# Kernel tuning notes

Measured on AMD Instinct MI355X. Metric: run time of the kernel, lower is better.

The kernel has to match this reference:

```python
import jax, jax.numpy as jnp
import numpy as np

THRESHOLD = 0.35      # overlap_thresh
NEGPOS_RATIO = 7
VAR0, VAR1 = 0.1, 0.2  # self.variance


def make_priors():
    # Standard RetinaFace 640x640 anchor grid -> 16800 priors (cx, cy, w, h)
    img = 640
    steps = [8, 16, 32]
    min_sizes = [[16, 32], [64, 128], [256, 512]]
    out = []
    for step, ms in zip(steps, min_sizes):
        f = img // step
        ii, jj = np.meshgrid(np.arange(f), np.arange(f), indexing="ij")
        cx = ((jj + 0.5) * step / img).ravel().astype(np.float32)
        cy = ((ii + 0.5) * step / img).ravel().astype(np.float32)
        for m in ms:
            s = np.full_like(cx, m / img)
            out.append(np.stack([cx, cy, s, s], axis=-1))
    return jnp.asarray(np.concatenate(out, axis=0), dtype=jnp.float32)


def jaccard(a, b):
    # a: [O,4] point-form gt boxes, b: [P,4] point-form priors -> IoU [O,P]
    lt = jnp.maximum(a[:, None, :2], b[None, :, :2])
    rb = jnp.minimum(a[:, None, 2:], b[None, :, 2:])
    wh = jnp.clip(rb - lt, 0.0)
    inter = wh[..., 0] * wh[..., 1]
    area_a = ((a[:, 2] - a[:, 0]) * (a[:, 3] - a[:, 1]))[:, None]
    area_b = ((b[:, 2] - b[:, 0]) * (b[:, 3] - b[:, 1]))[None, :]
    return inter / (area_a + area_b - inter)


def setup_inputs() -> dict:
    key = jax.random.key(0)
    ks = jax.random.split(key, 7)
    B, P, O = 64, 16800, 64
    loc_data = jax.random.normal(ks[0], (B, P, 4), jnp.float32)
    conf_data = jax.random.normal(ks[1], (B, P, 2), jnp.float32)
    landm_data = jax.random.normal(ks[2], (B, P, 10), jnp.float32)
    priors = make_priors()
    # targets: [B, O, 15] = [xmin ymin xmax ymax | 10 landmark coords | label]
    c = jax.random.uniform(ks[3], (B, O, 2), minval=0.15, maxval=0.85)
    wh = jax.random.uniform(ks[4], (B, O, 2), minval=0.05, maxval=0.3)
    boxes = jnp.concatenate([jnp.clip(c - wh / 2, 1e-3, 0.999),
                             jnp.clip(c + wh / 2, 1e-3, 0.999)], axis=-1)
    landms = jax.random.uniform(ks[5], (B, O, 10))
    lab = jnp.where(jax.random.uniform(ks[6], (B, O, 1)) < 0.8, 1.0, -1.0)
    targets = jnp.concatenate([boxes, landms, lab], axis=-1).astype(jnp.float32)
    return {"loc_data": loc_data, "conf_data": conf_data,
            "landm_data": landm_data, "priors": priors, "targets": targets}


def _smooth_l1(x):
    ax = jnp.abs(x)
    return jnp.where(ax < 1.0, 0.5 * ax * ax, ax - 0.5)


def reference(loc_data, conf_data, landm_data, priors, targets):
    B, P, C = conf_data.shape
    O = targets.shape[1]
    priors_pf = jnp.concatenate([priors[:, :2] - priors[:, 2:] * 0.5,
                                 priors[:, :2] + priors[:, 2:] * 0.5], axis=1)

    def match_one(t):
        truths = t[:, :4]
        landms = t[:, 4:14]
        labels = t[:, 14].astype(jnp.int32)
        ov = jaccard(truths, priors_pf)               # [O,P]
        bp_ov = ov.max(axis=1)                         # best prior per truth
        bp_idx = jnp.argmax(ov, axis=1)
        valid = bp_ov >= 0.2                           # RetinaFace gt filter
        bt_ov = ov.max(axis=0)                         # best truth per prior
        bt_idx = jnp.argmax(ov, axis=0)
        # index_fill_(best_prior_idx, 2) for valid gts, ensure best prior kept
        bt_ov = bt_ov.at[bp_idx].set(jnp.where(valid, 2.0, bt_ov[bp_idx]))
        bt_idx = bt_idx.at[bp_idx].set(jnp.arange(O))
        matched = truths[bt_idx]                       # [P,4] point form
        conf = labels[bt_idx]
        conf = jnp.where(bt_ov < THRESHOLD, 0, conf)
        # encode loc target
        g_cxcy = ((matched[:, :2] + matched[:, 2:]) * 0.5 - priors[:, :2]) / (VAR0 * priors[:, 2:])
        g_wh = jnp.log((matched[:, 2:] - matched[:, :2]) / priors[:, 2:]) / VAR1
        loc = jnp.concatenate([g_cxcy, g_wh], axis=1)
        # encode landmark target (5 points)
        ml = landms[bt_idx].reshape(P, 5, 2)
        lm = ((ml - priors[:, None, :2]) / (VAR0 * priors[:, None, 2:])).reshape(P, 10)
        any_valid = jnp.any(valid)                     # early-return branch of match()
        return (jnp.where(any_valid, loc, 0.0),
                jnp.where(any_valid, conf, 0),
                jnp.where(any_valid, lm, 0.0))

    loc_t, conf_t, landm_t = jax.vmap(match_one)(targets)
    loc_t = jax.lax.stop_gradient(loc_t)       # targets built from .data in torch
    landm_t = jax.lax.stop_gradient(landm_t)

    # landmark loss over conf_t > 0
    pos1 = conf_t > 0
    N1 = jnp.maximum(pos1.sum().astype(jnp.float32), 1.0)
    loss_landm = jnp.sum(jnp.where(pos1[..., None], _smooth_l1(landm_data - landm_t), 0.0))

    # localization loss over conf_t != 0 (labels -1 and 1 both positive)
    pos = conf_t != 0
    conf_t1 = jnp.where(pos, 1, conf_t)        # conf_t[pos] = 1 -> values in {0,1}
    loss_l = jnp.sum(jnp.where(pos[..., None], _smooth_l1(loc_data - loc_t), 0.0))

    # hard negative mining
    lse = jax.nn.logsumexp(conf_data, axis=2)                       # [B,P]
    picked = jnp.take_along_axis(conf_data, conf_t1[..., None], axis=2)[..., 0]
    ce_all = lse - picked                                            # per-anchor CE
    rank_score = jnp.where(pos, 0.0, ce_all)
    loss_idx = jnp.argsort(-rank_score, axis=1)
    idx_rank = jnp.argsort(loss_idx, axis=1)
    num_pos = pos.sum(axis=1, keepdims=True)
    num_neg = jnp.minimum(NEGPOS_RATIO * num_pos, P - 1)
    neg = idx_rank < num_neg
    union = pos | neg
    loss_c = jnp.sum(jnp.where(union, ce_all, 0.0))

    N = jnp.maximum(num_pos.sum().astype(jnp.float32), 1.0)
    return loss_l / N, loss_c / N, loss_landm / N1
```

## Files before the change

### kernel.cpp

```cpp
#include <hip/hip_runtime.h>
#include <math.h>

#define B 64
#define P 16800
#define O 64
#define THRESH 0.35f
#define VALID_T 0.2f
#define HB 2048
#define HSHIFT 21
#define AREA_M 0.34f
#define CCAP 4096
#define MULT 4
#define CHB (MULT * 256)
#define NB2 ((P + CHB - 1) / CHB)
#define KD1B (B * NB2)
#define KB2B (B * O / 4)

__device__ __forceinline__ float smooth_l1(float x) {
    float ax = fabsf(x);
    return ax < 1.f ? 0.5f * ax * ax : ax - 0.5f;
}
__device__ __forceinline__ float lse2(float c0, float c1) {
    float m = fmaxf(c0, c1);
    return m + __logf(__expf(c0 - m) + __expf(c1 - m));
}
__device__ __forceinline__ void iou_upd(float4 t, float area_a,
                                        float px1, float py1, float px2, float py2,
                                        float area_b,
                                        float& bnum, float& bden, int& bio, int o) {
    float w = fmaxf(fminf(t.z, px2) - fmaxf(t.x, px1), 0.f);
    float h = fmaxf(fminf(t.w, py2) - fmaxf(t.y, py1), 0.f);
    float inter = w * h;
    float den = area_a + area_b - inter;
    if (inter * bden > bnum * den) { bnum = inter; bden = den; bio = o; }
}
__device__ __forceinline__ float wave_sum(float v) {
#pragma unroll
    for (int s = 32; s > 0; s >>= 1) v += __shfl_down(v, s, 64);
    return v;
}
__device__ __forceinline__ int wave_sum_i(int v) {
#pragma unroll
    for (int s = 32; s > 0; s >>= 1) v += __shfl_down(v, s, 64);
    return v;
}
__device__ __forceinline__ float wave_min(float v) {
#pragma unroll
    for (int s = 32; s > 0; s >>= 1) v = fminf(v, __shfl_xor(v, s, 64));
    return v;
}
__device__ __forceinline__ float wave_max(float v) {
#pragma unroll
    for (int s = 32; s > 0; s >>= 1) v = fmaxf(v, __shfl_xor(v, s, 64));
    return v;
}
__device__ __forceinline__ int wave_sufscan(int v, int lane) {
#pragma unroll
    for (int s = 1; s < 64; s <<= 1) {
        int o = __shfl_down(v, s, 64);
        if (lane + s < 64) v += o;
    }
    return v;
}

__global__ void __launch_bounds__(256) kMain(
        const float* __restrict__ loc_data, const float* __restrict__ conf_data,
        const float* __restrict__ landm_data, const float* __restrict__ priors,
        const float* __restrict__ targets,
        float* __restrict__ rank,
        int* __restrict__ num_pos, float* __restrict__ pos_ce,
        float* __restrict__ gsum, int* __restrict__ np1_tot,
        unsigned long long* __restrict__ bp_final) {
    if (blockIdx.x >= KD1B) {
        int pair = (blockIdx.x - KD1B) * 4 + (threadIdx.x >> 6);
        int lane = threadIdx.x & 63;
        int o = pair & (O - 1);
        int b = pair >> 6;
        const float* tt = &targets[(b * O + o) * 15];
        float tx1 = tt[0], ty1 = tt[1], tx2 = tt[2], ty2 = tt[3];
        float area_a = (tx2 - tx1) * (ty2 - ty1);
        float4 tb = make_float4(tx1, ty1, tx2, ty2);
        float bn = 0.f, bd = 1.f;
        unsigned bp = 0u;
        const int fs[6]   = {80, 80, 40, 40, 20, 20};
        const int ms[6]   = {16, 32, 64, 128, 256, 512};
        const int base[6] = {0, 6400, 12800, 14400, 16000, 16400};
#pragma unroll
        for (int c = 0; c < 6; ++c) {
            int f = fs[c];
            float inv = (float)f;
            float h = (float)ms[c] * (0.5f / 640.f);
            int j0 = (int)floorf((tx1 - h) * inv - 0.5f) - 1; if (j0 < 0) j0 = 0;
            int j1 = (int)ceilf((tx2 + h) * inv - 0.5f) + 1;  if (j1 > f - 1) j1 = f - 1;
            int i0 = (int)floorf((ty1 - h) * inv - 0.5f) - 1; if (i0 < 0) i0 = 0;
            int i1 = (int)ceilf((ty2 + h) * inv - 0.5f) + 1;  if (i1 > f - 1) i1 = f - 1;
            if (j1 < j0 || i1 < i0) continue;
            int nj = j1 - j0 + 1;
            int n = (i1 - i0 + 1) * nj;
            float rcp_nj = 1.0f / (float)nj;
            for (int idx = lane; idx < n; idx += 64) {
                int ii = (int)((float)idx * rcp_nj);
                int jj = idx - ii * nj;
                if (jj < 0) { ii--; jj += nj; } else if (jj >= nj) { ii++; jj -= nj; }
                int p = base[c] + (i0 + ii) * f + (j0 + jj);
                float4 q = ((const float4*)priors)[p];
                float px1 = q.x - q.z * 0.5f, py1 = q.y - q.w * 0.5f;
                float px2 = q.x + q.z * 0.5f, py2 = q.y + q.w * 0.5f;
                float areab = (px2 - px1) * (py2 - py1);
                float w = fmaxf(fminf(tb.z, px2) - fmaxf(tb.x, px1), 0.f);
                float hh = fmaxf(fminf(tb.w, py2) - fmaxf(tb.y, py1), 0.f);
                float inter = w * hh;
                float den = area_a + areab - inter;
                float l = bn * den, r = inter * bd;
                if (r > l) { bn = inter; bd = den; bp = (unsigned)p; }
            }
        }
#pragma unroll
        for (int s = 32; s > 0; s >>= 1) {
            float no = __shfl_xor(bn, s, 64), dd = __shfl_xor(bd, s, 64);
            unsigned po = __shfl_xor(bp, s, 64);
            float l = bn * dd, r = no * bd;
            bool take = (r > l) || (r == l && po < bp);
            if (take) { bn = no; bd = dd; bp = po; }
        }
        if (lane == 0) {
            float iou = bn / bd;
            bp_final[b * O + o] = ((unsigned long long)__float_as_uint(iou) << 32)
                                | (unsigned)(0xFFFFFFFFu - bp);
        }
        return;
    }
    int blk = blockIdx.x % NB2;
    int b = blockIdx.x / NB2;
    int p0 = blk * CHB;
    __shared__ float traw[O * 15];
    __shared__ float4 t4[O];
    __shared__ float ta[O], lab[O];
    __shared__ float4 wbb[4];
    __shared__ float2 wab[4];
    __shared__ int alist[O];
    __shared__ int s_cnt;
    __shared__ float wredf[3][4];
    __shared__ int wredi[2][4];
    int tid = threadIdx.x;
    if (tid < O * 15 / 4)
        ((float4*)traw)[tid] = ((const float4*)(targets + (size_t)b * O * 15))[tid];
    float px1[MULT], py1[MULT], px2[MULT], py2[MULT], areab[MULT];
    float4 pr4[MULT];
    float bnum[MULT], bden[MULT]; int bi[MULT]; bool act[MULT];
    float bx1 = 1e30f, by1 = 1e30f, bx2 = -1e30f, by2 = -1e30f;
    float amn = 1e30f, amx = -1e30f;
#pragma unroll
    for (int mi = 0; mi < MULT; ++mi) {
        int p = p0 + mi * 256 + tid;
        act[mi] = (p < P);
        int pc = act[mi] ? p : (P - 1);
        float4 q = ((const float4*)priors)[pc];
        pr4[mi] = q;
        px1[mi] = q.x - q.z * 0.5f; py1[mi] = q.y - q.w * 0.5f;
        px2[mi] = q.x + q.z * 0.5f; py2[mi] = q.y + q.w * 0.5f;
        areab[mi] = (px2[mi] - px1[mi]) * (py2[mi] - py1[mi]);
        bx1 = fminf(bx1, px1[mi]); by1 = fminf(by1, py1[mi]);
        bx2 = fmaxf(bx2, px2[mi]); by2 = fmaxf(by2, py2[mi]);
        amn = fminf(amn, areab[mi]); amx = fmaxf(amx, areab[mi]);
        bnum[mi] = 0.f; bden[mi] = 1.f; bi[mi] = 0;
    }
    bx1 = wave_min(bx1); by1 = wave_min(by1);
    bx2 = wave_max(bx2); by2 = wave_max(by2);
    amn = wave_min(amn); amx = wave_max(amx);
    int wid = tid >> 6, lid = tid & 63;
    if (lid == 0) { wbb[wid] = make_float4(bx1, by1, bx2, by2); wab[wid] = make_float2(amn, amx); }
    __syncthreads();
    if (tid < 64) {
        const float* tr = &traw[tid * 15];
        float a0 = tr[0], a1 = tr[1], a2 = tr[2], a3 = tr[3];
        float4 t = make_float4(a0, a1, a2, a3);
        t4[tid] = t;
        float Aa = (a2 - a0) * (a3 - a1);
        ta[tid] = Aa;
        lab[tid] = tr[14];
        float ux1 = fminf(fminf(wbb[0].x, wbb[1].x), fminf(wbb[2].x, wbb[3].x));
        float uy1 = fminf(fminf(wbb[0].y, wbb[1].y), fminf(wbb[2].y, wbb[3].y));
        float ux2 = fmaxf(fmaxf(wbb[0].z, wbb[1].z), fmaxf(wbb[2].z, wbb[3].z));
        float uy2 = fmaxf(fmaxf(wbb[0].w, wbb[1].w), fmaxf(wbb[2].w, wbb[3].w));
        float bmn = fminf(fminf(wab[0].x, wab[1].x), fminf(wab[2].x, wab[3].x));
        float bmx = fmaxf(fmaxf(wab[0].y, wab[1].y), fmaxf(wab[2].y, wab[3].y));
        bool pass = (fminf(t.z, ux2) - fmaxf(t.x, ux1) > 0.f) &&
                    (fminf(t.w, uy2) - fmaxf(t.y, uy1) > 0.f) &&
                    (Aa >= AREA_M * bmn) && (bmx >= AREA_M * Aa);
        unsigned long long mask = __ballot(pass);
        if (tid == 0) s_cnt = __popcll(mask);
        if (pass) {
            int pos = __popcll(mask & ((1ull << tid) - 1ull));
            alist[pos] = tid;
        }
    }
    __syncthreads();
    int cnt = s_cnt;
    for (int li = 0; li < cnt; ++li) {
        int o = alist[li];
        float4 t = t4[o];
        float w0 = fminf(t.z, bx2) - fmaxf(t.x, bx1);
        float h0 = fminf(t.w, by2) - fmaxf(t.y, by1);
        if (w0 <= 0.f || h0 <= 0.f) continue;
        float Aa = ta[o];
#pragma unroll
        for (int mi = 0; mi < MULT; ++mi) {
            float Ap = areab[mi];
            if (Aa >= AREA_M * Ap && Ap >= AREA_M * Aa)
                iou_upd(t, Aa, px1[mi], py1[mi], px2[mi], py2[mi], Ap,
                        bnum[mi], bden[mi], bi[mi], o);
        }
    }
    float ll = 0.f, llm = 0.f, cep = 0.f;
    int cp = 0, cp1 = 0;
#pragma unroll
    for (int mi = 0; mi < MULT; ++mi) {
        if (!act[mi]) continue;
        int p = p0 + mi * 256 + tid;
        float best = bnum[mi] / bden[mi];
        int conf = (best >= THRESH) ? (int)lab[bi[mi]] : 0;
        float2 c01 = ((const float2*)conf_data)[b * P + p];
        float c0 = c01.x, c1 = c01.y;
        float lse = lse2(c0, c1);
        bool pos = conf != 0;
        float ce = lse - (pos ? c1 : c0);
        float rv = pos ? 0.f : ce;
        rank[(size_t)b * P + p] = rv;
        if (pos) {
            cp++; cep += ce;
            int ti = bi[mi];
            float cx = pr4[mi].x, cy = pr4[mi].y, sw = pr4[mi].z, sh = pr4[mi].w;
            float4 t = t4[ti];
            float gx = ((t.x + t.z) * 0.5f - cx) / (0.1f * sw);
            float gy = ((t.y + t.w) * 0.5f - cy) / (0.1f * sh);
            float gw = logf((t.z - t.x) / sw) / 0.2f;
            float gh = logf((t.w - t.y) / sh) / 0.2f;
            const float* ld = &loc_data[(size_t)(b * P + p) * 4];
            ll += smooth_l1(ld[0] - gx) + smooth_l1(ld[1] - gy) +
                  smooth_l1(ld[2] - gw) + smooth_l1(ld[3] - gh);
            if (conf > 0) {
                cp1++;
                const float* lmd = &landm_data[(size_t)(b * P + p) * 10];
                const float* lmt = &traw[ti * 15 + 4];
                for (int k5 = 0; k5 < 5; ++k5) {
                    float lx = (lmt[k5 * 2 + 0] - cx) / (0.1f * sw);
                    float ly = (lmt[k5 * 2 + 1] - cy) / (0.1f * sh);
                    llm += smooth_l1(lmd[k5 * 2 + 0] - lx) + smooth_l1(lmd[k5 * 2 + 1] - ly);
                }
            }
        }
    }
    float s_ll = wave_sum(ll), s_llm = wave_sum(llm), s_cep = wave_sum(cep);
    int s_cp = wave_sum_i(cp), s_cp1 = wave_sum_i(cp1);
    if (lid == 0) {
        wredf[0][wid] = s_ll; wredf[1][wid] = s_llm; wredf[2][wid] = s_cep;
        wredi[0][wid] = s_cp; wredi[1][wid] = s_cp1;
    }
    __syncthreads();
    if (tid == 0) {
        float ll_t = wredf[0][0] + wredf[0][1] + wredf[0][2] + wredf[0][3];
        float llm_t = wredf[1][0] + wredf[1][1] + wredf[1][2] + wredf[1][3];
        float cep_t = wredf[2][0] + wredf[2][1] + wredf[2][2] + wredf[2][3];
        int cp_t = wredi[0][0] + wredi[0][1] + wredi[0][2] + wredi[0][3];
        int cp1_t = wredi[1][0] + wredi[1][1] + wredi[1][2] + wredi[1][3];
        if (ll_t != 0.f)  atomicAdd(&gsum[0], ll_t);
        if (llm_t != 0.f) atomicAdd(&gsum[1], llm_t);
        if (cep_t != 0.f) atomicAdd(&pos_ce[b], cep_t);
        if (cp_t)  atomicAdd(&num_pos[b], cp_t);
        if (cp1_t) atomicAdd(np1_tot, cp1_t);
    }
}

__global__ void __launch_bounds__(1024) kTail(
        const float* __restrict__ priors, const float* __restrict__ targets,
        const float* __restrict__ loc_data, const float* __restrict__ conf_data,
        const float* __restrict__ landm_data,
        const unsigned long long* __restrict__ bp_final,
        const float* __restrict__ rank,
        const int* __restrict__ num_pos, const float* __restrict__ pos_ce,
        float* __restrict__ gsum, int* __restrict__ np1_tot, int* __restrict__ np_tot,
        float* __restrict__ lossc_tot, int* __restrict__ done,
        float* __restrict__ out) {
    __shared__ __align__(16) unsigned lrow[P];
    __shared__ float4 t4[O];
    __shared__ float ta[O], lab[O];
    __shared__ int sp[O];
    __shared__ int lh[HB];
    __shared__ int chunkSum[256];
    __shared__ int suf[257];
    __shared__ int waveTot[4];
    __shared__ int hist2[256];
    __shared__ unsigned lcand[CCAP];
    __shared__ int s_np, s_bin0, s_kk0, s_bin, s_kk, s_cnt;
    __shared__ float wredf[16];
    __shared__ int wredi[16];
    __shared__ float s_sumgt;

    int b = blockIdx.x;
    int tid = threadIdx.x;
    const float* r = rank + (size_t)b * P;
    for (int i = tid; i < HB; i += 1024) lh[i] = 0;
    if (tid == 0) s_cnt = 0;
    int p = 0, v = 0;
    if (tid < O) {
        const float* tt = &targets[(b * O + tid) * 15];
        float4 tj = make_float4(tt[0], tt[1], tt[2], tt[3]);
        t4[tid] = tj;
        ta[tid] = (tj.z - tj.x) * (tj.w - tj.y);
        lab[tid] = tt[14];
        unsigned long long kpk = bp_final[b * O + tid];
        p = (int)(0xFFFFFFFFu - (unsigned)(kpk & 0xFFFFFFFFu));
        float iou = __uint_as_float((unsigned)(kpk >> 32));
        v = (iou >= VALID_T) ? 1 : 0;
        sp[tid] = p;
    }
    __syncthreads();
    const float4* r4 = (const float4*)r;
    for (int i = tid; i < P / 4; i += 1024) {
        float4 q = r4[i];
        uint4 u = make_uint4(__float_as_uint(q.x), __float_as_uint(q.y),
                             __float_as_uint(q.z), __float_as_uint(q.w));
        ((uint4*)lrow)[i] = u;
        atomicAdd(&lh[u.x >> HSHIFT], 1);
        atomicAdd(&lh[u.y >> HSHIFT], 1);
        atomicAdd(&lh[u.z >> HSHIFT], 1);
        atomicAdd(&lh[u.w >> HSHIFT], 1);
    }
    __syncthreads();
    int dnp = 0, dn1 = 0;
    float dll = 0.f, dllm = 0.f, dce = 0.f;
    if (tid < O) {
        int j = tid;
        bool winner = true;
        for (int jj = j + 1; jj < O; ++jj)
            if (sp[jj] == p) { winner = false; break; }
        if (winner) {
            float4 q = ((const float4*)priors)[p];
            float px1 = q.x - q.z * 0.5f, py1 = q.y - q.w * 0.5f;
            float px2 = q.x + q.z * 0.5f, py2 = q.y + q.w * 0.5f;
            float areab = (px2 - px1) * (py2 - py1);
            float bnum = 0.f, bden = 1.f; int bi = 0;
            for (int o = 0; o < O; ++o) {
                float Aa = ta[o];
                if (Aa >= AREA_M * areab && areab >= AREA_M * Aa)
                    iou_upd(t4[o], Aa, px1, py1, px2, py2, areab, bnum, bden, bi, o);
            }
            float best = bnum / bden;
            float ov_new = v ? 2.0f : best;
            int conf_old = (best >= THRESH) ? (int)lab[bi] : 0;
            int conf_new = (ov_new >= THRESH) ? (int)lab[j] : 0;
            float2 c01 = ((const float2*)conf_data)[b * P + p];
            float c0 = c01.x, c1 = c01.y;
            float lse = lse2(c0, c1);
            bool po = conf_old != 0, pn = conf_new != 0;
            float ceo = lse - (po ? c1 : c0), cen = lse - (pn ? c1 : c0);
            float rvo = po ? 0.f : ceo, rvn = pn ? 0.f : cen;
            if (__float_as_uint(rvo) != __float_as_uint(rvn)) {
                lrow[p] = __float_as_uint(rvn);
                int bo = __float_as_uint(rvo) >> HSHIFT, bn = __float_as_uint(rvn) >> HSHIFT;
                if (bo != bn) { atomicAdd(&lh[bn], 1); atomicAdd(&lh[bo], -1); }
            }
            const float* ld = &loc_data[(size_t)(b * P + p) * 4];
            auto enc_ll = [&](int ti) -> float {
                float4 t = t4[ti];
                float gx = ((t.x + t.z) * 0.5f - q.x) / (0.1f * q.z);
                float gy = ((t.y + t.w) * 0.5f - q.y) / (0.1f * q.w);
                float gw = logf((t.z - t.x) / q.z) / 0.2f;
                float gh = logf((t.w - t.y) / q.w) / 0.2f;
                return smooth_l1(ld[0] - gx) + smooth_l1(ld[1] - gy) +
                       smooth_l1(ld[2] - gw) + smooth_l1(ld[3] - gh);
            };
            if (po) dll -= enc_ll(bi);
            if (pn) dll += enc_ll(j);
            dce = (pn ? cen : 0.f) - (po ? ceo : 0.f);
            dnp = (int)pn - (int)po;
            const float* lmd = &landm_data[(size_t)(b * P + p) * 10];
            auto enc_lm = [&](int ti) -> float {
                const float* lmt = &targets[(b * O + ti) * 15 + 4];
                float sum = 0.f;
                for (int k5 = 0; k5 < 5; ++k5) {
                    float lx = (lmt[k5 * 2 + 0] - q.x) / (0.1f * q.z);
                    float ly = (lmt[k5 * 2 + 1] - q.y) / (0.1f * q.w);
                    sum += smooth_l1(lmd[k5 * 2 + 0] - lx) + smooth_l1(lmd[k5 * 2 + 1] - ly);
                }
                return sum;
            };
            if (conf_old > 0) dllm -= enc_lm(bi);
            if (conf_new > 0) dllm += enc_lm(j);
            dn1 = (int)(conf_new > 0) - (int)(conf_old > 0);
        }
    }
    float pce_reg = 0.f;
    if (tid < 64) {
        float r_ll = wave_sum(dll), r_lm = wave_sum(dllm), r_ce = wave_sum(dce);
        int r_np = wave_sum_i(dnp), r_n1 = wave_sum_i(dn1);
        if (tid == 0) {
            if (r_ll != 0.f) atomicAdd(&gsum[0], r_ll);
            if (r_lm != 0.f) atomicAdd(&gsum[1], r_lm);
            pce_reg = pos_ce[b] + r_ce;
            int np = num_pos[b] + r_np;
            s_np = np;
            atomicAdd(np_tot, np);
            if (r_n1) atomicAdd(np1_tot, r_n1);
        }
    }
    __syncthreads();
    int k = s_np * 7;
    if (k > P - 1) k = P - 1;
    if (tid < 256) {
        int cs = 0;
#pragma unroll
        for (int i = 0; i < HB / 256; ++i) cs += lh[tid * (HB / 256) + i];
        chunkSum[tid] = cs;
    }
    if (tid == 0) { s_bin0 = (k <= 0) ? -1 : 0; s_kk0 = (k <= 0) ? 0 : k; }
    __syncthreads();
    {
        int lane = tid & 63;
        int vv = (tid < 256) ? chunkSum[tid] : 0;
        vv = wave_sufscan(vv, lane);
        if (tid < 256 && lane == 0) waveTot[tid >> 6] = vv;
        __syncthreads();
        if (tid < 256) {
            int after = 0;
            for (int g = (tid >> 6) + 1; g < 4; ++g) after += waveTot[g];
            suf[tid] = vv + after;
            if (tid == 0) suf[256] = 0;
        }
        __syncthreads();
        if (k > 0 && tid < 256) {
            if (suf[tid] >= k && suf[tid + 1] < k) {
                int cum = suf[tid + 1];
                for (int i = HB / 256 - 1; i >= 0; --i) {
                    int hv = lh[tid * (HB / 256) + i];
                    if (cum + hv >= k) { s_bin0 = tid * (HB / 256) + i; s_kk0 = k - cum; break; }
                    cum += hv;
                }
            }
        }
    }
    __syncthreads();
    int bin = s_bin0;
    int kk0 = s_kk0;
    float topk_b = 0.f;
    if (bin >= 0) {
        if (tid < 256) hist2[tid] = 0;
        __syncthreads();
        unsigned lo_bound = ((unsigned)(bin + 1)) << HSHIFT;
        float sumgt = 0.f;
        for (int i = tid; i < P / 4; i += 1024) {
            uint4 u4 = ((const uint4*)lrow)[i];
#define TAIL_H(u) { if ((u) >= lo_bound) sumgt += __uint_as_float(u); \
                    else if (((u) >> HSHIFT) == (unsigned)bin) { \
                        int idx = atomicAdd(&s_cnt, 1); \
                        if (idx < CCAP) lcand[idx] = (u); \
                        atomicAdd(&hist2[((u) >> 13) & 255], 1); } }
            TAIL_H(u4.x) TAIL_H(u4.y) TAIL_H(u4.z) TAIL_H(u4.w)
#undef TAIL_H
        }
        float sg = wave_sum(sumgt);
        if ((tid & 63) == 0) wredf[tid >> 6] = sg;
        __syncthreads();
        if (tid == 0) {
            float t = 0.f;
            for (int i = 0; i < 16; ++i) t += wredf[i];
            s_sumgt = t;
        }
        {
            int lane = tid & 63, nb = 256;
            int vv = (tid < nb) ? hist2[tid] : 0;
            vv = wave_sufscan(vv, lane);
            if (tid < nb && lane == 0) waveTot[tid >> 6] = vv;
            __syncthreads();
            if (tid < nb) {
                int after = 0;
                for (int g = (tid >> 6) + 1; g < 4; ++g) after += waveTot[g];
                suf[tid] = vv + after;
                if (tid == 0) suf[nb] = 0;
            }
            __syncthreads();
            if (tid < nb) {
                if (suf[tid] >= kk0 && suf[tid + 1] < kk0) { s_bin = tid; s_kk = kk0 - suf[tid + 1]; }
            }
            __syncthreads();
        }
        unsigned pref = (((unsigned)bin) << HSHIFT) | (((unsigned)s_bin) << 13);
        unsigned resolved = (0xFFFFFFFFu << HSHIFT) | (255u << 13);
        int kk = s_kk;
        int m = s_cnt;
        bool useG = (m > CCAP);
        for (int pass = 0; pass < 2; ++pass) {
            int sh = pass == 0 ? 5 : 0;
            int nb = pass == 0 ? 256 : 32;
            if (tid < nb) hist2[tid] = 0;
            __syncthreads();
            if (!useG) {
                for (int i = tid; i < m; i += 1024) {
                    unsigned u = lcand[i];
                    if ((u & resolved) == pref) atomicAdd(&hist2[(u >> sh) & (nb - 1)], 1);
                }
            } else {
                for (int pp = tid; pp < P; pp += 1024) {
                    unsigned u = lrow[pp];
                    if ((u & resolved) == pref) atomicAdd(&hist2[(u >> sh) & (nb - 1)], 1);
                }
            }
            __syncthreads();
            {
                int lane = tid & 63;
                int vv = (tid < nb) ? hist2[tid] : 0;
                vv = wave_sufscan(vv, lane);
                if (tid < nb && lane == 0) waveTot[tid >> 6] = vv;
                __syncthreads();
                int ng = (nb + 63) >> 6;
                if (tid < nb) {
                    int after = 0;
                    for (int g = (tid >> 6) + 1; g < ng; ++g) after += waveTot[g];
                    suf[tid] = vv + after;
                    if (tid == 0) suf[nb] = 0;
                }
                __syncthreads();
                if (tid < nb) {
                    if (suf[tid] >= kk && suf[tid + 1] < kk) { s_bin = tid; s_kk = kk - suf[tid + 1]; }
                }
                __syncthreads();
            }
            pref |= ((unsigned)s_bin) << sh;
            resolved |= (unsigned)(nb - 1) << sh;
            kk = s_kk;
            __syncthreads();
        }
        float tv = __uint_as_float(pref);
        float sumS = 0.f; int cntS = 0;
        for (int pp = tid; pp < P; pp += 1024) {
            unsigned u = lrow[pp];
            if ((u >> HSHIFT) == (unsigned)bin) {
                float val = __uint_as_float(u);
                if (val > tv) { sumS += val; cntS++; }
            }
        }
        float s2 = wave_sum(sumS); int c2 = wave_sum_i(cntS);
        if ((tid & 63) == 0) { wredf[tid >> 6] = s2; wredi[tid >> 6] = c2; }
        __syncthreads();
        if (tid == 0) {
            float st = 0.f; int ct = 0;
            for (int i = 0; i < 16; ++i) { st += wredf[i]; ct += wredi[i]; }
            topk_b = s_sumgt + st + (float)(kk0 - ct) * tv;
        }
    }
    if (tid == 0) {
        atomicAdd(lossc_tot, pce_reg + topk_b);
        __threadfence();
        int old = atomicAdd(done, 1);
        if (old == B - 1) {
            float g0 = atomicAdd(&gsum[0], 0.f);
            float g1 = atomicAdd(&gsum[1], 0.f);
            float lc = atomicAdd(lossc_tot, 0.f);
            int np = atomicAdd(np_tot, 0);
            int n1 = atomicAdd(np1_tot, 0);
            float N = fmaxf((float)np, 1.f);
            float N1 = fmaxf((float)n1, 1.f);
            out[0] = g0 / N;
            out[1] = lc / N;
            out[2] = g1 / N1;
        }
    }
}

extern "C" void kernel_launch(void* const* d_in, const int* in_sizes, int n_in,
                              void* d_out, int out_size, void* d_ws, size_t ws_size,
                              hipStream_t stream) {
    const float* loc_data   = (const float*)d_in[0];
    const float* conf_data  = (const float*)d_in[1];
    const float* landm_data = (const float*)d_in[2];
    const float* priors     = (const float*)d_in[3];
    const float* targets    = (const float*)d_in[4];
    float* out = (float*)d_out;

    char* ws = (char*)d_ws;
    size_t off = 0;
    auto alloc = [&](size_t bytes) -> void* {
        void* pp = ws + off;
        off += (bytes + 255) & ~(size_t)255;
        return pp;
    };
    float* rank     = (float*)alloc((size_t)B * P * 4);
    unsigned long long* bp_final = (unsigned long long*)alloc((size_t)B * O * 8);
    size_t acc_bytes = (size_t)(2 * B * 4 + 64);
    char* acc = (char*)alloc(acc_bytes);
    int*   num_pos      = (int*)acc;
    float* pos_ce       = (float*)(acc + B * 4);
    float* gsum         = (float*)(acc + 2 * B * 4);
    int*   np1_tot      = (int*)(acc + 2 * B * 4 + 8);
    int*   np_tot       = (int*)(acc + 2 * B * 4 + 12);
    float* lossc_tot    = (float*)(acc + 2 * B * 4 + 16);
    int*   done         = (int*)(acc + 2 * B * 4 + 20);

    hipMemsetAsync(acc, 0, acc_bytes, stream);
    kMain<<<dim3(KD1B + KB2B), dim3(256), 0, stream>>>(loc_data, conf_data, landm_data,
                                                       priors, targets, rank,
                                                       num_pos, pos_ce, gsum, np1_tot,
                                                       bp_final);
    kTail<<<dim3(B), dim3(1024), 0, stream>>>(priors, targets, loc_data, conf_data,
                                              landm_data, bp_final, rank,
                                              num_pos, pos_ce, gsum, np1_tot, np_tot,
                                              lossc_tot, done, out);
}
```

Baseline: 170.9 us.

## Write byte positive flags in main kernel and compute CE in tail

The main kernel no longer reads conf_data or writes a float rank array. It writes a one-byte positive flag per anchor instead. The tail kernel reads conf_data directly, computes the log-sum-exp cross-entropy, builds the rank row and histogram, and sums positive CE locally, which replaces the pos_ce atomics. MULT is also halved to 2, doubling the main kernel's block count. This cuts the intermediate global traffic from 4 bytes to 1 byte per anchor, but the CE work moves into the tail's 64 blocks, which have less parallelism.

```diff
diff --git a/kernel.cpp b/kernel.cpp
--- a/kernel.cpp
+++ b/kernel.cpp
@@ -10,7 +10,7 @@
 #define HSHIFT 21
 #define AREA_M 0.34f
 #define CCAP 4096
-#define MULT 4
+#define MULT 2
 #define CHB (MULT * 256)
 #define NB2 ((P + CHB - 1) / CHB)
 #define KD1B (B * NB2)
@@ -64,11 +64,11 @@
 }
 
 __global__ void __launch_bounds__(256) kMain(
-        const float* __restrict__ loc_data, const float* __restrict__ conf_data,
+        const float* __restrict__ loc_data,
         const float* __restrict__ landm_data, const float* __restrict__ priors,
         const float* __restrict__ targets,
-        float* __restrict__ rank,
-        int* __restrict__ num_pos, float* __restrict__ pos_ce,
+        unsigned char* __restrict__ pflag,
+        int* __restrict__ num_pos,
         float* __restrict__ gsum, int* __restrict__ np1_tot,
         unsigned long long* __restrict__ bp_final) {
     if (blockIdx.x >= KD1B) {
@@ -140,7 +140,7 @@
     __shared__ float2 wab[4];
     __shared__ int alist[O];
     __shared__ int s_cnt;
-    __shared__ float wredf[3][4];
+    __shared__ float wredf[2][4];
     __shared__ int wredi[2][4];
     int tid = threadIdx.x;
     if (tid < O * 15 / 4)
@@ -212,7 +212,7 @@
                         bnum[mi], bden[mi], bi[mi], o);
         }
     }
-    float ll = 0.f, llm = 0.f, cep = 0.f;
+    float ll = 0.f, llm = 0.f;
     int cp = 0, cp1 = 0;
 #pragma unroll
     for (int mi = 0; mi < MULT; ++mi) {
@@ -220,15 +220,10 @@
         int p = p0 + mi * 256 + tid;
         float best = bnum[mi] / bden[mi];
         int conf = (best >= THRESH) ? (int)lab[bi[mi]] : 0;
-        float2 c01 = ((const float2*)conf_data)[b * P + p];
-        float c0 = c01.x, c1 = c01.y;
-        float lse = lse2(c0, c1);
         bool pos = conf != 0;
-        float ce = lse - (pos ? c1 : c0);
-        float rv = pos ? 0.f : ce;
-        rank[(size_t)b * P + p] = rv;
+        pflag[(size_t)b * P + p] = pos ? 1 : 0;
         if (pos) {
-            cp++; cep += ce;
+            cp++;
             int ti = bi[mi];
             float cx = pr4[mi].x, cy = pr4[mi].y, sw = pr4[mi].z, sh = pr4[mi].w;
             float4 t = t4[ti];
@@ -251,22 +246,20 @@
             }
         }
     }
-    float s_ll = wave_sum(ll), s_llm = wave_sum(llm), s_cep = wave_sum(cep);
+    float s_ll = wave_sum(ll), s_llm = wave_sum(llm);
     int s_cp = wave_sum_i(cp), s_cp1 = wave_sum_i(cp1);
     if (lid == 0) {
-        wredf[0][wid] = s_ll; wredf[1][wid] = s_llm; wredf[2][wid] = s_cep;
+        wredf[0][wid] = s_ll; wredf[1][wid] = s_llm;
         wredi[0][wid] = s_cp; wredi[1][wid] = s_cp1;
     }
     __syncthreads();
     if (tid == 0) {
         float ll_t = wredf[0][0] + wredf[0][1] + wredf[0][2] + wredf[0][3];
         float llm_t = wredf[1][0] + wredf[1][1] + wredf[1][2] + wredf[1][3];
-        float cep_t = wredf[2][0] + wredf[2][1] + wredf[2][2] + wredf[2][3];
         int cp_t = wredi[0][0] + wredi[0][1] + wredi[0][2] + wredi[0][3];
         int cp1_t = wredi[1][0] + wredi[1][1] + wredi[1][2] + wredi[1][3];
         if (ll_t != 0.f)  atomicAdd(&gsum[0], ll_t);
         if (llm_t != 0.f) atomicAdd(&gsum[1], llm_t);
-        if (cep_t != 0.f) atomicAdd(&pos_ce[b], cep_t);
         if (cp_t)  atomicAdd(&num_pos[b], cp_t);
         if (cp1_t) atomicAdd(np1_tot, cp1_t);
     }
@@ -277,8 +270,8 @@
         const float* __restrict__ loc_data, const float* __restrict__ conf_data,
         const float* __restrict__ landm_data,
         const unsigned long long* __restrict__ bp_final,
-        const float* __restrict__ rank,
-        const int* __restrict__ num_pos, const float* __restrict__ pos_ce,
+        const unsigned char* __restrict__ pflag,
+        const int* __restrict__ num_pos,
         float* __restrict__ gsum, int* __restrict__ np1_tot, int* __restrict__ np_tot,
         float* __restrict__ lossc_tot, int* __restrict__ done,
         float* __restrict__ out) {
@@ -295,11 +288,11 @@
     __shared__ int s_np, s_bin0, s_kk0, s_bin, s_kk, s_cnt;
     __shared__ float wredf[16];
     __shared__ int wredi[16];
+    __shared__ float s_cepw[16];
     __shared__ float s_sumgt;
 
     int b = blockIdx.x;
     int tid = threadIdx.x;
-    const float* r = rank + (size_t)b * P;
     for (int i = tid; i < HB; i += 1024) lh[i] = 0;
     if (tid == 0) s_cnt = 0;
     int p = 0, v = 0;
@@ -316,16 +309,37 @@
         sp[tid] = p;
     }
     __syncthreads();
-    const float4* r4 = (const float4*)r;
+    const float4* c4 = (const float4*)(conf_data + (size_t)b * P * 2);
+    const uchar4* f4v = (const uchar4*)(pflag + (size_t)b * P);
+    float cep = 0.f;
     for (int i = tid; i < P / 4; i += 1024) {
-        float4 q = r4[i];
-        uint4 u = make_uint4(__float_as_uint(q.x), __float_as_uint(q.y),
-                             __float_as_uint(q.z), __float_as_uint(q.w));
-        ((uint4*)lrow)[i] = u;
-        atomicAdd(&lh[u.x >> HSHIFT], 1);
-        atomicAdd(&lh[u.y >> HSHIFT], 1);
-        atomicAdd(&lh[u.z >> HSHIFT], 1);
-        atomicAdd(&lh[u.w >> HSHIFT], 1);
+        float4 a = c4[2 * i];
+        float4 c = c4[2 * i + 1];
+        uchar4 fl = f4v[i];
+        float l0 = lse2(a.x, a.y), l1 = lse2(a.z, a.w);
+        float l2 = lse2(c.x, c.y), l3 = lse2(c.z, c.w);
+        bool q0 = fl.x != 0, q1 = fl.y != 0, q2 = fl.z != 0, q3 = fl.w != 0;
+        float ce0 = l0 - (q0 ? a.y : a.x);
+        float ce1 = l1 - (q1 ? a.w : a.z);
+        float ce2 = l2 - (q2 ? c.y : c.x);
+        float ce3 = l3 - (q3 ? c.w : c.z);
+        if (q0) cep += ce0;
+        if (q1) cep += ce1;
+        if (q2) cep += ce2;
+        if (q3) cep += ce3;
+        unsigned u0 = __float_as_uint(q0 ? 0.f : ce0);
+        unsigned u1 = __float_as_uint(q1 ? 0.f : ce1);
+        unsigned u2 = __float_as_uint(q2 ? 0.f : ce2);
+        unsigned u3 = __float_as_uint(q3 ? 0.f : ce3);
+        ((uint4*)lrow)[i] = make_uint4(u0, u1, u2, u3);
+        atomicAdd(&lh[u0 >> HSHIFT], 1);
+        atomicAdd(&lh[u1 >> HSHIFT], 1);
+        atomicAdd(&lh[u2 >> HSHIFT], 1);
+        atomicAdd(&lh[u3 >> HSHIFT], 1);
+    }
+    {
+        float sc = wave_sum(cep);
+        if ((tid & 63) == 0) s_cepw[tid >> 6] = sc;
     }
     __syncthreads();
     int dnp = 0, dn1 = 0;
@@ -398,7 +412,9 @@
         if (tid == 0) {
             if (r_ll != 0.f) atomicAdd(&gsum[0], r_ll);
             if (r_lm != 0.f) atomicAdd(&gsum[1], r_lm);
-            pce_reg = pos_ce[b] + r_ce;
+            float cep_tot = 0.f;
+            for (int i = 0; i < 16; ++i) cep_tot += s_cepw[i];
+            pce_reg = cep_tot + r_ce;
             int np = num_pos[b] + r_np;
             s_np = np;
             atomicAdd(np_tot, np);
@@ -585,25 +601,24 @@
         off += (bytes + 255) & ~(size_t)255;
         return pp;
     };
-    float* rank     = (float*)alloc((size_t)B * P * 4);
+    unsigned char* pflag = (unsigned char*)alloc((size_t)B * P);
     unsigned long long* bp_final = (unsigned long long*)alloc((size_t)B * O * 8);
-    size_t acc_bytes = (size_t)(2 * B * 4 + 64);
+    size_t acc_bytes = (size_t)(B * 4 + 64);
     char* acc = (char*)alloc(acc_bytes);
     int*   num_pos      = (int*)acc;
-    float* pos_ce       = (float*)(acc + B * 4);
-    float* gsum         = (float*)(acc + 2 * B * 4);
-    int*   np1_tot      = (int*)(acc + 2 * B * 4 + 8);
-    int*   np_tot       = (int*)(acc + 2 * B * 4 + 12);
-    float* lossc_tot    = (float*)(acc + 2 * B * 4 + 16);
-    int*   done         = (int*)(acc + 2 * B * 4 + 20);
+    float* gsum         = (float*)(acc + B * 4);
+    int*   np1_tot      = (int*)(acc + B * 4 + 8);
+    int*   np_tot       = (int*)(acc + B * 4 + 12);
+    float* lossc_tot    = (float*)(acc + B * 4 + 16);
+    int*   done         = (int*)(acc + B * 4 + 20);
 
     hipMemsetAsync(acc, 0, acc_bytes, stream);
-    kMain<<<dim3(KD1B + KB2B), dim3(256), 0, stream>>>(loc_data, conf_data, landm_data,
-                                                       priors, targets, rank,
-                                                       num_pos, pos_ce, gsum, np1_tot,
+    kMain<<<dim3(KD1B + KB2B), dim3(256), 0, stream>>>(loc_data, landm_data,
+                                                       priors, targets, pflag,
+                                                       num_pos, gsum, np1_tot,
                                                        bp_final);
     kTail<<<dim3(B), dim3(1024), 0, stream>>>(priors, targets, loc_data, conf_data,
-                                              landm_data, bp_final, rank,
-                                              num_pos, pos_ce, gsum, np1_tot, np_tot,
+                                              landm_data, bp_final, pflag,
+                                              num_pos, gsum, np1_tot, np_tot,
                                               lossc_tot, done, out);
 }
```

Result: faster. 165.4 us (-3.2%).
